# Performance work log

Hardware: AMD Instinct MI355X
Metric: run time of the kernel (lower is better)

Reference implementation:

```python
import jax, jax.numpy as jnp
import numpy as np

D = 512; H = 8; NL = 8; V = 258; W = 8; DFF = 4 * D; DH = D // H


def setup_inputs() -> dict:
    key = jax.random.key(0)
    ks = jax.random.split(key, 20)
    B, L = 8, 1024
    s = 0.02
    n = lambda k, shp: (jax.random.normal(k, shp, jnp.float32) * s)
    x = jax.random.randint(ks[0], (B, L), 0, 256)
    return dict(
        x=x,
        embed=n(ks[1], (V, D)),
        ep_w=n(ks[2], (D, 1)), ep_b=jnp.zeros((D,), jnp.float32),
        in_w=n(ks[3], (NL, 3 * D, D)), in_b=jnp.zeros((NL, 3 * D), jnp.float32),
        op_w=n(ks[4], (NL, D, D)), op_b=jnp.zeros((NL, D), jnp.float32),
        ln1_w=jnp.ones((NL, D), jnp.float32), ln1_b=jnp.zeros((NL, D), jnp.float32),
        ln2_w=jnp.ones((NL, D), jnp.float32), ln2_b=jnp.zeros((NL, D), jnp.float32),
        f1_w=n(ks[5], (NL, DFF, D)), f1_b=jnp.zeros((NL, DFF), jnp.float32),
        f2_w=n(ks[6], (NL, D, DFF)), f2_b=jnp.zeros((NL, D), jnp.float32),
        out_w=n(ks[7], (V, D)),
    )


def _layer_norm(x, w, b, eps=1e-5):
    mu = jnp.mean(x, -1, keepdims=True)
    var = jnp.mean(jnp.square(x - mu), -1, keepdims=True)
    return (x - mu) * jax.lax.rsqrt(var + eps) * w + b


def _entropy_features(x):
    # Sliding-window byte histogram entropy (same math as one-hot.sum over window)
    B, L = x.shape
    oh = jax.nn.one_hot(x, V, dtype=jnp.float32)          # [B,L,V]
    oh = oh.at[..., 256:].set(0.0)                        # special tokens zeroed
    cs = jnp.cumsum(oh, axis=1)
    cs = jnp.concatenate([jnp.zeros_like(cs[:, :1]), cs], axis=1)
    counts = cs[:, W:] - cs[:, :-W]                       # [B, L-W+1, V]
    probs = jnp.clip(counts / W, 1e-10)
    ent = -jnp.sum(probs * (jnp.log(probs) / jnp.log(2.0)), -1, keepdims=True)
    return jnp.pad(ent, ((0, 0), (0, W - 1), (0, 0)))     # [B,L,1]


def _block(h, in_w, in_b, op_w, op_b, ln1_w, ln1_b, ln2_w, ln2_b, f1_w, f1_b, f2_w, f2_b):
    B, L, _ = h.shape
    g = _layer_norm(h, ln1_w, ln1_b)
    qkv = g @ in_w.T + in_b                               # [B,L,3D]
    q, k, v = jnp.split(qkv, 3, axis=-1)
    q = q.reshape(B, L, H, DH); k = k.reshape(B, L, H, DH); v = v.reshape(B, L, H, DH)
    scores = jnp.einsum('blhd,bmhd->bhlm', q, k) / np.sqrt(DH).astype(np.float32)
    attn = jax.nn.softmax(scores, axis=-1)
    o = jnp.einsum('bhlm,bmhd->blhd', attn, v).reshape(B, L, D)
    h = h + o @ op_w.T + op_b
    g = _layer_norm(h, ln2_w, ln2_b)
    h = h + jax.nn.gelu(g @ f1_w.T + f1_b, approximate=False) @ f2_w.T + f2_b
    return h


def reference(x, embed, ep_w, ep_b, in_w, in_b, op_w, op_b, ln1_w, ln1_b,
              ln2_w, ln2_b, f1_w, f1_b, f2_w, f2_b, out_w):
    ent = _entropy_features(x)                            # [B,L,1]
    h = embed[x] + ent @ ep_w.T + ep_b                    # [B,L,D]
    for i in range(NL // 2):                              # local encoder layers
        h = _block(h, in_w[i], in_b[i], op_w[i], op_b[i], ln1_w[i], ln1_b[i],
                   ln2_w[i], ln2_b[i], f1_w[i], f1_b[i], f2_w[i], f2_b[i])
    for i in range(NL // 2, NL):                          # global transformer layers
        h = _block(h, in_w[i], in_b[i], op_w[i], op_b[i], ln1_w[i], ln1_b[i],
                   ln2_w[i], ln2_b[i], f1_w[i], f1_b[i], f2_w[i], f2_b[i])
    return h @ out_w.T                                    # [B,L,V]
```

## Files before the change

### kernel.cpp

```cpp
#include <hip/hip_runtime.h>
#include <hip/hip_bf16.h>

#define D_MODEL 512
#define NHEAD   8
#define DHEAD   64
#define SEQ     1024
#define NBATCH  8
#define NTOK    8192
#define DFF_N   2048
#define NLAYER  8
#define VOCAB   258
#define VPAD    384

typedef float f32x4 __attribute__((ext_vector_type(4)));
typedef short s16x8 __attribute__((ext_vector_type(8)));

__device__ __forceinline__ ushort f2b(float f) {
    union { float f; unsigned u; } v; v.f = f;
    unsigned r = (v.u + 0x7fffu + ((v.u >> 16) & 1u)) >> 16;
    return (ushort)r;
}
__device__ __forceinline__ float gelu_f(float x) {
    return 0.5f * x * (1.0f + erff(x * 0.70710678118654752f));
}
__device__ __forceinline__ void gl_lds16(const void* g, void* l) {
    __builtin_amdgcn_global_load_lds(
        (const __attribute__((address_space(1))) void*)g,
        (__attribute__((address_space(3))) void*)l, 16, 0, 0);
}
__device__ __forceinline__ float exp2_fast(float x) {
    float r; asm("v_exp_f32 %0, %1" : "=v"(r) : "v"(x)); return r;
}
__device__ __forceinline__ unsigned cvtpk(float lo, float hi) {
    unsigned r; asm("v_cvt_pk_bf16_f32 %0, %1, %2" : "=v"(r) : "v"(lo), "v"(hi)); return r;
}

__global__ __launch_bounds__(256) void cvt_bf16(
    const float* __restrict__ in, ushort* __restrict__ out, int n)
{
    int i = (blockIdx.x * 256 + threadIdx.x) << 2;
    if (i >= n) return;
    float4 v = *(const float4*)(in + i);
    ushort4 o;
    o.x = f2b(v.x); o.y = f2b(v.y); o.z = f2b(v.z); o.w = f2b(v.w);
    *(ushort4*)(out + i) = o;
}

__global__ __launch_bounds__(256) void cvt_layer(
    const float* __restrict__ s0, const float* __restrict__ s1,
    const float* __restrict__ s2, const float* __restrict__ s3,
    ushort* __restrict__ d0, ushort* __restrict__ d1,
    ushort* __restrict__ d2, ushort* __restrict__ d3)
{
    int i = (blockIdx.x * 256 + threadIdx.x) << 2;
    const float* s; ushort* d; int off;
    if (i < 786432)        { s = s0; d = d0; off = i; }
    else if (i < 1048576)  { s = s1; d = d1; off = i - 786432; }
    else if (i < 2097152)  { s = s2; d = d2; off = i - 1048576; }
    else                   { s = s3; d = d3; off = i - 2097152; }
    float4 v = *(const float4*)(s + off);
    ushort4 o;
    o.x = f2b(v.x); o.y = f2b(v.y); o.z = f2b(v.z); o.w = f2b(v.w);
    *(ushort4*)(d + off) = o;
}

__global__ __launch_bounds__(128) void embed_kernel(
    const int* __restrict__ x, const float* __restrict__ embed,
    const float* __restrict__ ep_w, const float* __restrict__ ep_b,
    float* __restrict__ h)
{
    int t = blockIdx.x;
    int pos = t & (SEQ - 1);
    float ent = 0.0f;
    if (pos <= SEQ - 8) {
        int v[8];
        #pragma unroll
        for (int i = 0; i < 8; i++) v[i] = x[t + i];
        float s = 0.0f;
        #pragma unroll
        for (int i = 0; i < 8; i++) {
            int c = 0;
            #pragma unroll
            for (int j = 0; j < 8; j++) c += (v[j] == v[i]) ? 1 : 0;
            s += log2f((float)c);
        }
        ent = 3.0f - 0.125f * s;
    }
    int tok = x[t];
    int d = threadIdx.x << 2;
    float e[4], w[4], bb[4], r[4];
    *(float4*)e  = *(const float4*)(embed + (size_t)tok * D_MODEL + d);
    *(float4*)w  = *(const float4*)(ep_w + d);
    *(float4*)bb = *(const float4*)(ep_b + d);
    #pragma unroll
    for (int j = 0; j < 4; j++) r[j] = e[j] + ent * w[j] + bb[j];
    *(float4*)(h + (size_t)t * D_MODEL + d) = *(float4*)r;
}

__global__ __launch_bounds__(256) void ln_kernel(
    const float* __restrict__ in, const float* __restrict__ w,
    const float* __restrict__ b, ushort* __restrict__ out)
{
    int wid = threadIdx.x >> 6, lane = threadIdx.x & 63;
    int t = (blockIdx.x << 2) + wid;
    const float* row = in + (size_t)t * D_MODEL;
    float a[8];
    *(float4*)(a)     = *(const float4*)(row + (lane << 2));
    *(float4*)(a + 4) = *(const float4*)(row + 256 + (lane << 2));
    float s = 0.f;
    #pragma unroll
    for (int j = 0; j < 8; j++) s += a[j];
    #pragma unroll
    for (int o = 1; o < 64; o <<= 1) s += __shfl_xor(s, o);
    float mu = s * (1.0f / 512.0f);
    float vs = 0.f;
    #pragma unroll
    for (int j = 0; j < 8; j++) { float d0 = a[j] - mu; vs += d0 * d0; }
    #pragma unroll
    for (int o = 1; o < 64; o <<= 1) vs += __shfl_xor(vs, o);
    float inv = rsqrtf(vs * (1.0f / 512.0f) + 1e-5f);
    float ww[8], bbv[8];
    *(float4*)(ww)      = *(const float4*)(w + (lane << 2));
    *(float4*)(ww + 4)  = *(const float4*)(w + 256 + (lane << 2));
    *(float4*)(bbv)     = *(const float4*)(b + (lane << 2));
    *(float4*)(bbv + 4) = *(const float4*)(b + 256 + (lane << 2));
    ushort* orow = out + (size_t)t * D_MODEL;
    ushort4 o1, o2;
    o1.x = f2b((a[0] - mu) * inv * ww[0] + bbv[0]);
    o1.y = f2b((a[1] - mu) * inv * ww[1] + bbv[1]);
    o1.z = f2b((a[2] - mu) * inv * ww[2] + bbv[2]);
    o1.w = f2b((a[3] - mu) * inv * ww[3] + bbv[3]);
    o2.x = f2b((a[4] - mu) * inv * ww[4] + bbv[4]);
    o2.y = f2b((a[5] - mu) * inv * ww[5] + bbv[5]);
    o2.z = f2b((a[6] - mu) * inv * ww[6] + bbv[6]);
    o2.w = f2b((a[7] - mu) * inv * ww[7] + bbv[7]);
    *(ushort4*)(orow + (lane << 2))       = o1;
    *(ushort4*)(orow + 256 + (lane << 2)) = o2;
}

template<int BN>
__global__ __launch_bounds__(256) void gemm_t(
    const ushort* __restrict__ A, const ushort* __restrict__ Bw,
    const float* __restrict__ bias, const float* __restrict__ resid,
    float* __restrict__ Cf, ushort* __restrict__ Cb, ushort* __restrict__ Vtr,
    int M, int N, int K, int fuse)
{
    constexpr int NF = BN / 32;
    constexpr int EPW = BN + 4;
    __shared__ ushort SMEM[3 * 4096 + 3 * BN * 32];
    ushort* As0 = SMEM;
    ushort* Bs0 = SMEM + 12288;
    const int tid = threadIdx.x;
    const int l = tid & 63, w = tid >> 6;
    const int p  = blockIdx.y * gridDim.x + blockIdx.x;
    const int bx = ((p & 7) << 3) + ((p >> 3) & 7);
    const int by = p >> 6;
    const int m0 = bx << 7, n0 = by * BN;
    const int wrn = (w >> 1) << 6;
    const int wcn = (w & 1) * (BN / 2);
    const int fm = l & 15;
    const int soff = (((l & 3) ^ ((l >> 3) & 3)) << 3);
    const int foff = (((l >> 4) ^ ((fm >> 1) & 3)) << 3);
    f32x4 acc[4][NF] = {};

    const ushort* ga0 = A + (size_t)(m0 + (w << 5) + (l >> 2)) * K + soff;
    const ushort* ga1 = ga0 + (size_t)16 * K;
    const ushort* gb0;
    const ushort* gb1 = nullptr;
    if constexpr (BN == 128) {
        gb0 = Bw + (size_t)(n0 + (w << 5) + (l >> 2)) * K + soff;
        gb1 = gb0 + (size_t)16 * K;
    } else {
        gb0 = Bw + (size_t)(n0 + (w << 4) + (l >> 2)) * K + soff;
    }

    const int nk = K >> 5;
    auto stage = [&](int buf, int ko) {
        gl_lds16(ga0 + ko, As0 + buf * 4096 + (w << 10));
        gl_lds16(ga1 + ko, As0 + buf * 4096 + (w << 10) + 512);
        if constexpr (BN == 128) {
            gl_lds16(gb0 + ko, Bs0 + buf * (BN * 32) + (w << 10));
            gl_lds16(gb1 + ko, Bs0 + buf * (BN * 32) + (w << 10) + 512);
        } else {
            gl_lds16(gb0 + ko, Bs0 + buf * (BN * 32) + (w << 9));
        }
    };

    stage(0, 0);
    stage(1, 32);
    int cur = 0;
    for (int kt = 0; kt < nk; ++kt) {
        if (kt + 1 < nk) {
            if constexpr (BN == 128) asm volatile("s_waitcnt vmcnt(4)" ::: "memory");
            else                     asm volatile("s_waitcnt vmcnt(3)" ::: "memory");
        } else {
            asm volatile("s_waitcnt vmcnt(0)" ::: "memory");
        }
        asm volatile("s_barrier" ::: "memory");
        __builtin_amdgcn_sched_barrier(0);
        {
            int nxt = cur + 2; if (nxt >= 3) nxt -= 3;
            if (kt + 2 < nk) stage(nxt, (kt + 2) << 5);
        }
        s16x8 af[4], bf[NF];
        #pragma unroll
        for (int x = 0; x < 4; ++x)
            af[x] = *(const s16x8*)&As0[cur * 4096 + (wrn + (x << 4) + fm) * 32 + foff];
        #pragma unroll
        for (int y = 0; y < NF; ++y)
            bf[y] = *(const s16x8*)&Bs0[cur * (BN * 32) + (wcn + (y << 4) + fm) * 32 + foff];
        #pragma unroll
        for (int x = 0; x < 4; ++x)
            #pragma unroll
            for (int y = 0; y < NF; ++y)
                acc[x][y] = __builtin_amdgcn_mfma_f32_16x16x32_bf16(
                    af[x], bf[y], acc[x][y], 0, 0, 0);
        cur = (cur == 2) ? 0 : cur + 1;
    }
    __syncthreads();

    const float qs = (Vtr && n0 < 512) ? 0.18033688011112042f : 1.0f;
    const bool vblk = (Vtr != nullptr) && (n0 >= 1024);

    if (Cb != nullptr || vblk) {
        float* Ep = (float*)SMEM;
        const int lrw = ((w >> 1) << 4) + ((l >> 4) << 2);
        #pragma unroll
        for (int x = 0; x < 4; ++x) {
            __syncthreads();
            #pragma unroll
            for (int y = 0; y < NF; ++y) {
                const int c = wcn + (y << 4) + fm;
                const float bv = bias ? bias[n0 + c] : 0.f;
                #pragma unroll
                for (int i = 0; i < 4; ++i) {
                    float v = acc[x][y][i] + bv;
                    v *= qs;
                    if (fuse == 1) v = gelu_f(v);
                    Ep[(lrw + i) * EPW + c] = v;
                }
            }
            __syncthreads();
            if (vblk) {
                const int c = tid & 127;
                const int run = tid >> 7;
                const int colg = (n0 - 1024) + c;
                const int hh = colg >> 6, dd = colg & 63;
                float v16[16];
                #pragma unroll
                for (int j = 0; j < 16; ++j)
                    v16[j] = Ep[((run << 4) + j) * EPW + c];
                unsigned pk[8];
                #pragma unroll
                for (int j = 0; j < 8; ++j) pk[j] = cvtpk(v16[2 * j], v16[2 * j + 1]);
                ushort* dst = Vtr + ((size_t)(((m0 >> 10) << 3) + hh) * 64 + dd) * 1024
                              + (m0 & 1023) + (run << 6) + (x << 4);
                *(uint4*)dst       = *(uint4*)(pk);
                *(uint4*)(dst + 8) = *(uint4*)(pk + 4);
            } else {
                constexpr int TPR = BN / 8;
                constexpr int RPP = 256 / TPR;
                constexpr int NP = 32 / RPP;
                #pragma unroll
                for (int p2 = 0; p2 < NP; ++p2) {
                    const int lr = p2 * RPP + (tid / TPR);
                    const int cg = (tid % TPR) << 3;
                    const int grow = m0 + ((lr >> 4) << 6) + (x << 4) + (lr & 15);
                    const int gcol = n0 + cg;
                    float v8[8];
                    *(float4*)(v8)     = *(float4*)&Ep[lr * EPW + cg];
                    *(float4*)(v8 + 4) = *(float4*)&Ep[lr * EPW + cg + 4];
                    if (fuse == 2) {
                        float4 r1 = *(const float4*)&resid[(size_t)grow * N + gcol];
                        float4 r2 = *(const float4*)&resid[(size_t)grow * N + gcol + 4];
                        v8[0] += r1.x; v8[1] += r1.y; v8[2] += r1.z; v8[3] += r1.w;
                        v8[4] += r2.x; v8[5] += r2.y; v8[6] += r2.z; v8[7] += r2.w;
                    }
                    if (Cf) {
                        *(float4*)&Cf[(size_t)grow * N + gcol]     = *(float4*)v8;
                        *(float4*)&Cf[(size_t)grow * N + gcol + 4] = *(float4*)(v8 + 4);
                    }
                    unsigned pk[4];
                    pk[0] = cvtpk(v8[0], v8[1]); pk[1] = cvtpk(v8[2], v8[3]);
                    pk[2] = cvtpk(v8[4], v8[5]); pk[3] = cvtpk(v8[6], v8[7]);
                    *(uint4*)&Cb[(size_t)grow * N + gcol] = *(uint4*)pk;
                }
            }
        }
        return;
    }

    const int col0 = n0 + wcn + fm;
    const int row0 = m0 + wrn + ((l >> 4) << 2);
    #pragma unroll
    for (int x = 0; x < 4; ++x) {
        #pragma unroll
        for (int y = 0; y < NF; ++y) {
            int col = col0 + (y << 4);
            if (col >= N) continue;
            float bv = bias ? bias[col] : 0.f;
            #pragma unroll
            for (int i = 0; i < 4; ++i) {
                int row = row0 + (x << 4) + i;
                float v = acc[x][y][i] + bv;
                if (fuse == 1) v = gelu_f(v);
                else if (fuse == 2) v += resid[(size_t)row * N + col];
                Cf[(size_t)row * N + col] = v;
            }
        }
    }
}

__global__ __launch_bounds__(512) void attn_mfma(
    const ushort* __restrict__ qkv, const ushort* __restrict__ vT,
    ushort* __restrict__ out)
{
    __shared__ ushort Ks[2][4096];
    __shared__ ushort Vs[2][4096];
    const int tid = threadIdx.x;
    const int l = tid & 63, w = tid >> 6;
    const int p = blockIdx.y * gridDim.x + blockIdx.x;
    const int bh = ((p & 7) << 3) + (p >> 6);
    const int q0 = ((p >> 3) & 7) << 7;
    const int b = bh >> 3, h = bh & 7;
    const ushort* base = qkv + (size_t)b * SEQ * 1536 + h * 64;
    const ushort* kg = base + 512;
    const ushort* vg = vT + ((size_t)bh << 16);
    const int fm = l & 15, fk = l >> 4;

    s16x8 qf[2];
    {
        const ushort* qrow = base + (size_t)(q0 + (w << 4) + fm) * 1536 + (fk << 3);
        qf[0] = *(const s16x8*)qrow;
        qf[1] = *(const s16x8*)(qrow + 32);
    }
    s16x8 ones_f;
    #pragma unroll
    for (int j = 0; j < 8; ++j) ones_f[j] = (short)0x3F80;

    f32x4 accO[4] = {};
    f32x4 accL = {};

    const int srow = (w << 3) + (l >> 3);
    const int cch = ((l & 7) ^ (l >> 3)) << 3;
    const ushort* kga = kg + (size_t)srow * 1536 + cch;
    const ushort* vga = vg + (size_t)srow * 1024 + cch;

    int fidx[2][4];
    #pragma unroll
    for (int ks = 0; ks < 2; ++ks)
        #pragma unroll
        for (int n = 0; n < 4; ++n)
            fidx[ks][n] = (((n << 4) + fm) << 6) + ((((ks << 2) + fk) ^ (l & 7)) << 3);

    const int srcA = ((fk & 1) << 5) + fm;
    const int srcB = srcA + 16;
    const bool hiN = (fk >> 1) != 0;

    #define STAGE(buf, kt)                                                    \
        do {                                                                  \
            gl_lds16(kga + (size_t)((kt) << 6) * 1536, &Ks[buf][w << 9]);     \
            gl_lds16(vga + ((kt) << 6), &Vs[buf][w << 9]);                    \
        } while (0)

    STAGE(0, 0);
    asm volatile("s_waitcnt vmcnt(0)" ::: "memory");
    __builtin_amdgcn_s_barrier();

    int cur = 0;
    for (int kt = 0; kt < SEQ / 64; ++kt) {
        if (kt + 1 < SEQ / 64) STAGE(cur ^ 1, kt + 1);
        __builtin_amdgcn_sched_barrier(0);

        f32x4 s[4] = {};
        __builtin_amdgcn_s_setprio(1);
        #pragma unroll
        for (int ks = 0; ks < 2; ++ks)
            #pragma unroll
            for (int n = 0; n < 4; ++n) {
                s16x8 kf = *(const s16x8*)&Ks[cur][fidx[ks][n]];
                s[n] = __builtin_amdgcn_mfma_f32_16x16x32_bf16(kf, qf[ks], s[n], 0, 0, 0);
            }
        __builtin_amdgcn_s_setprio(0);

        unsigned pk0[2], pk1[2], pk2[2], pk3[2];
        pk0[0] = cvtpk(exp2_fast(s[0][0]), exp2_fast(s[0][1]));
        pk0[1] = cvtpk(exp2_fast(s[0][2]), exp2_fast(s[0][3]));
        pk1[0] = cvtpk(exp2_fast(s[1][0]), exp2_fast(s[1][1]));
        pk1[1] = cvtpk(exp2_fast(s[1][2]), exp2_fast(s[1][3]));
        pk2[0] = cvtpk(exp2_fast(s[2][0]), exp2_fast(s[2][1]));
        pk2[1] = cvtpk(exp2_fast(s[2][2]), exp2_fast(s[2][3]));
        pk3[0] = cvtpk(exp2_fast(s[3][0]), exp2_fast(s[3][1]));
        pk3[1] = cvtpk(exp2_fast(s[3][2]), exp2_fast(s[3][3]));

        #pragma unroll
        for (int ks = 0; ks < 2; ++ks) {
            unsigned u0 = ks ? pk2[0] : pk0[0], u1 = ks ? pk2[1] : pk0[1];
            unsigned v0 = ks ? pk3[0] : pk1[0], v1 = ks ? pk3[1] : pk1[1];
            unsigned a0 = __shfl((int)u0, srcA), b0 = __shfl((int)v0, srcA);
            unsigned a1 = __shfl((int)u1, srcA), b1 = __shfl((int)v1, srcA);
            unsigned a2 = __shfl((int)u0, srcB), b2 = __shfl((int)v0, srcB);
            unsigned a3 = __shfl((int)u1, srcB), b3 = __shfl((int)v1, srcB);
            union { unsigned u[4]; s16x8 v; } pb;
            pb.u[0] = hiN ? b0 : a0;
            pb.u[1] = hiN ? b1 : a1;
            pb.u[2] = hiN ? b2 : a2;
            pb.u[3] = hiN ? b3 : a3;
            __builtin_amdgcn_s_setprio(1);
            #pragma unroll
            for (int n = 0; n < 4; ++n) {
                s16x8 vf = *(const s16x8*)&Vs[cur][fidx[ks][n]];
                accO[n] = __builtin_amdgcn_mfma_f32_16x16x32_bf16(vf, pb.v, accO[n], 0, 0, 0);
            }
            accL = __builtin_amdgcn_mfma_f32_16x16x32_bf16(ones_f, pb.v, accL, 0, 0, 0);
            __builtin_amdgcn_s_setprio(0);
        }

        asm volatile("s_waitcnt vmcnt(0)" ::: "memory");
        __builtin_amdgcn_s_barrier();
        __builtin_amdgcn_sched_barrier(0);
        cur ^= 1;
    }
    #undef STAGE

    const int q = q0 + (w << 4) + fm;
    float inv = 1.0f / accL[0];
    ushort* obase = out + ((size_t)(b * SEQ + q)) * 512 + h * 64 + (fk << 2);
    #pragma unroll
    for (int n = 0; n < 4; ++n) {
        ushort4 o;
        o.x = f2b(accO[n][0] * inv);
        o.y = f2b(accO[n][1] * inv);
        o.z = f2b(accO[n][2] * inv);
        o.w = f2b(accO[n][3] * inv);
        *(ushort4*)(obase + (n << 4)) = o;
    }
}

extern "C" void kernel_launch(void* const* d_in, const int* in_sizes, int n_in,
                              void* d_out, int out_size, void* d_ws, size_t ws_size,
                              hipStream_t stream) {
    const int*   x     = (const int*)  d_in[0];
    const float* embed = (const float*)d_in[1];
    const float* ep_w  = (const float*)d_in[2];
    const float* ep_b  = (const float*)d_in[3];
    const float* in_w  = (const float*)d_in[4];
    const float* in_b  = (const float*)d_in[5];
    const float* op_w  = (const float*)d_in[6];
    const float* op_b  = (const float*)d_in[7];
    const float* ln1_w = (const float*)d_in[8];
    const float* ln1_b = (const float*)d_in[9];
    const float* ln2_w = (const float*)d_in[10];
    const float* ln2_b = (const float*)d_in[11];
    const float* f1_w  = (const float*)d_in[12];
    const float* f1_b  = (const float*)d_in[13];
    const float* f2_w  = (const float*)d_in[14];
    const float* f2_b  = (const float*)d_in[15];
    const float* out_w = (const float*)d_in[16];
    float* out = (float*)d_out;

    char* ws = (char*)d_ws;
    float*  h    = (float*) (ws + 0);
    ushort* g    = (ushort*)(ws + 16777216);
    ushort* big  = (ushort*)(ws + 25165824);
    ushort* qkvb = big;
    ushort* hb   = (ushort*)(ws + 58720256);
    ushort* wq   = (ushort*)(ws + 67108864);
    ushort* wo   = (ushort*)(ws + 68681728);
    ushort* w1   = (ushort*)(ws + 69206016);
    ushort* w2   = (ushort*)(ws + 71303168);
    ushort* wv   = (ushort*)(ws + 73400320);
    ushort* vT   = (ushort*)(ws + 73793536);

    hipMemsetAsync(wv, 0, (size_t)VPAD * 512 * 2, stream);
    cvt_bf16<<<(VOCAB * 512 / 4 + 255) / 256, 256, 0, stream>>>(out_w, wv, VOCAB * 512);

    embed_kernel<<<NTOK, 128, 0, stream>>>(x, embed, ep_w, ep_b, h);

    for (int l = 0; l < NLAYER; ++l) {
        cvt_layer<<<3072, 256, 0, stream>>>(
            in_w + (size_t)l * 786432, op_w + (size_t)l * 262144,
            f1_w + (size_t)l * 1048576, f2_w + (size_t)l * 1048576,
            wq, wo, w1, w2);

        ln_kernel<<<NTOK / 4, 256, 0, stream>>>(h, ln1_w + l * 512, ln1_b + l * 512, g);
        gemm_t<128><<<dim3(64, 12), 256, 0, stream>>>(g, wq, in_b + l * 1536, nullptr,
                                                      nullptr, qkvb, vT, NTOK, 1536, 512, 0);
        attn_mfma<<<dim3(SEQ / 128, 64), 512, 0, stream>>>(qkvb, vT, g);
        gemm_t<64><<<dim3(64, 8), 256, 0, stream>>>(g, wo, op_b + l * 512, h,
                                                    h, nullptr, nullptr, NTOK, 512, 512, 2);
        ln_kernel<<<NTOK / 4, 256, 0, stream>>>(h, ln2_w + l * 512, ln2_b + l * 512, g);
        gemm_t<128><<<dim3(64, 16), 256, 0, stream>>>(g, w1, f1_b + l * 2048, nullptr,
                                                      nullptr, big, nullptr, NTOK, 2048, 512, 1);
        gemm_t<64><<<dim3(64, 8), 256, 0, stream>>>(big, w2, f2_b + l * 512, h,
                                                    h, (l == NLAYER - 1) ? hb : nullptr, nullptr,
                                                    NTOK, 512, 2048, 2);
    }

    gemm_t<64><<<dim3(64, 5), 256, 0, stream>>>(hb, wv, nullptr, nullptr,
                                                out, nullptr, nullptr, NTOK, VOCAB, 512, 0);
}
```

Before: 1.351 ms.

## Add triple-buffered BK=64 GEMM kernel for N=512 projections and output head

Introduces a new 128x64-tile GEMM that stages 64-wide K slices into a three-deep LDS ring with async global-to-LDS loads and XOR-swizzled addressing. Each barrier now covers two MFMA k-steps, and loads run two tiles ahead. It replaces the older 64-variant GEMM for the attention out-projection, the FFN down-projection and the vocab head. The bf16 output path stages results through LDS for vectorized stores. The cost is more LDS per block, which may reduce occupancy.

After: 1.297 ms, median of 2. -4.0%, faster.

```diff
diff --git a/kernel.cpp b/kernel.cpp
--- a/kernel.cpp
+++ b/kernel.cpp
@@ -311,6 +311,159 @@
     }
 }
 
+__global__ __launch_bounds__(256) void gemm_k64(
+    const ushort* __restrict__ A, const ushort* __restrict__ Bw,
+    const float* __restrict__ bias, const float* __restrict__ resid,
+    float* __restrict__ Cf, ushort* __restrict__ Cb,
+    int M, int N, int K, int fuse)
+{
+    constexpr int EPW = 68;
+    __shared__ ushort SMEM[3 * 8192 + 3 * 4096];
+    ushort* As0 = SMEM;
+    ushort* Bs0 = SMEM + 24576;
+    const int tid = threadIdx.x;
+    const int l = tid & 63, w = tid >> 6;
+    const int p  = blockIdx.y * gridDim.x + blockIdx.x;
+    const int bx = ((p & 7) << 3) + ((p >> 3) & 7);
+    const int by = p >> 6;
+    const int m0 = bx << 7, n0 = by << 6;
+    const int wrn = (w >> 1) << 6;
+    const int wcn = (w & 1) << 5;
+    const int fm = l & 15, fk = l >> 4;
+    f32x4 acc[4][2] = {};
+
+    const int srow = (w << 3) + (l >> 3);
+    const int cch = ((l & 7) ^ (l >> 3)) << 3;
+    const ushort* gaP0 = A + (size_t)(m0 + srow) * K + cch;
+    const ushort* gbP0 = Bw + (size_t)(n0 + srow) * K + cch;
+
+    const int foff0 = (((0 << 2) + fk) ^ (fm & 7)) << 3;
+    const int foff1 = (((1 << 2) + fk) ^ (fm & 7)) << 3;
+
+    const int nk = K >> 6;
+    auto stage = [&](int buf, int ko) {
+        #pragma unroll
+        for (int p2 = 0; p2 < 4; ++p2)
+            gl_lds16(gaP0 + (size_t)(p2 << 5) * K + ko,
+                     As0 + buf * 8192 + (p2 << 11) + (w << 9));
+        #pragma unroll
+        for (int p2 = 0; p2 < 2; ++p2)
+            gl_lds16(gbP0 + (size_t)(p2 << 5) * K + ko,
+                     Bs0 + buf * 4096 + (p2 << 11) + (w << 9));
+    };
+
+    stage(0, 0);
+    stage(1, 64);
+    int cur = 0;
+    for (int kt = 0; kt < nk; ++kt) {
+        if (kt + 1 < nk) asm volatile("s_waitcnt vmcnt(6)" ::: "memory");
+        else             asm volatile("s_waitcnt vmcnt(0)" ::: "memory");
+        asm volatile("s_barrier" ::: "memory");
+        __builtin_amdgcn_sched_barrier(0);
+        {
+            int nxt = cur + 2; if (nxt >= 3) nxt -= 3;
+            if (kt + 2 < nk) stage(nxt, (kt + 2) << 6);
+        }
+        {
+            s16x8 af[4], bf[2];
+            #pragma unroll
+            for (int x = 0; x < 4; ++x)
+                af[x] = *(const s16x8*)&As0[cur * 8192 + (wrn + (x << 4) + fm) * 64 + foff0];
+            #pragma unroll
+            for (int y = 0; y < 2; ++y)
+                bf[y] = *(const s16x8*)&Bs0[cur * 4096 + (wcn + (y << 4) + fm) * 64 + foff0];
+            #pragma unroll
+            for (int x = 0; x < 4; ++x)
+                #pragma unroll
+                for (int y = 0; y < 2; ++y)
+                    acc[x][y] = __builtin_amdgcn_mfma_f32_16x16x32_bf16(
+                        af[x], bf[y], acc[x][y], 0, 0, 0);
+        }
+        {
+            s16x8 af[4], bf[2];
+            #pragma unroll
+            for (int x = 0; x < 4; ++x)
+                af[x] = *(const s16x8*)&As0[cur * 8192 + (wrn + (x << 4) + fm) * 64 + foff1];
+            #pragma unroll
+            for (int y = 0; y < 2; ++y)
+                bf[y] = *(const s16x8*)&Bs0[cur * 4096 + (wcn + (y << 4) + fm) * 64 + foff1];
+            #pragma unroll
+            for (int x = 0; x < 4; ++x)
+                #pragma unroll
+                for (int y = 0; y < 2; ++y)
+                    acc[x][y] = __builtin_amdgcn_mfma_f32_16x16x32_bf16(
+                        af[x], bf[y], acc[x][y], 0, 0, 0);
+        }
+        cur = (cur == 2) ? 0 : cur + 1;
+    }
+    __syncthreads();
+
+    if (Cb != nullptr) {
+        float* Ep = (float*)SMEM;
+        const int lrw = ((w >> 1) << 4) + ((l >> 4) << 2);
+        #pragma unroll
+        for (int x = 0; x < 4; ++x) {
+            __syncthreads();
+            #pragma unroll
+            for (int y = 0; y < 2; ++y) {
+                const int c = wcn + (y << 4) + fm;
+                const float bv = bias ? bias[n0 + c] : 0.f;
+                #pragma unroll
+                for (int i = 0; i < 4; ++i) {
+                    float v = acc[x][y][i] + bv;
+                    if (fuse == 1) v = gelu_f(v);
+                    Ep[(lrw + i) * EPW + c] = v;
+                }
+            }
+            __syncthreads();
+            {
+                const int lr = tid >> 3;
+                const int cg = (tid & 7) << 3;
+                const int grow = m0 + ((lr >> 4) << 6) + (x << 4) + (lr & 15);
+                const int gcol = n0 + cg;
+                float v8[8];
+                *(float4*)(v8)     = *(float4*)&Ep[lr * EPW + cg];
+                *(float4*)(v8 + 4) = *(float4*)&Ep[lr * EPW + cg + 4];
+                if (fuse == 2) {
+                    float4 r1 = *(const float4*)&resid[(size_t)grow * N + gcol];
+                    float4 r2 = *(const float4*)&resid[(size_t)grow * N + gcol + 4];
+                    v8[0] += r1.x; v8[1] += r1.y; v8[2] += r1.z; v8[3] += r1.w;
+                    v8[4] += r2.x; v8[5] += r2.y; v8[6] += r2.z; v8[7] += r2.w;
+                }
+                if (Cf) {
+                    *(float4*)&Cf[(size_t)grow * N + gcol]     = *(float4*)v8;
+                    *(float4*)&Cf[(size_t)grow * N + gcol + 4] = *(float4*)(v8 + 4);
+                }
+                unsigned pk[4];
+                pk[0] = cvtpk(v8[0], v8[1]); pk[1] = cvtpk(v8[2], v8[3]);
+                pk[2] = cvtpk(v8[4], v8[5]); pk[3] = cvtpk(v8[6], v8[7]);
+                *(uint4*)&Cb[(size_t)grow * N + gcol] = *(uint4*)pk;
+            }
+        }
+        return;
+    }
+
+    const int col0 = n0 + wcn + fm;
+    const int row0 = m0 + wrn + ((l >> 4) << 2);
+    #pragma unroll
+    for (int x = 0; x < 4; ++x) {
+        #pragma unroll
+        for (int y = 0; y < 2; ++y) {
+            int col = col0 + (y << 4);
+            if (col >= N) continue;
+            float bv = bias ? bias[col] : 0.f;
+            #pragma unroll
+            for (int i = 0; i < 4; ++i) {
+                int row = row0 + (x << 4) + i;
+                float v = acc[x][y][i] + bv;
+                if (fuse == 1) v = gelu_f(v);
+                else if (fuse == 2) v += resid[(size_t)row * N + col];
+                Cf[(size_t)row * N + col] = v;
+            }
+        }
+    }
+}
+
 __global__ __launch_bounds__(512) void attn_mfma(
     const ushort* __restrict__ qkv, const ushort* __restrict__ vT,
     ushort* __restrict__ out)
@@ -487,16 +640,16 @@
         gemm_t<128><<<dim3(64, 12), 256, 0, stream>>>(g, wq, in_b + l * 1536, nullptr,
                                                       nullptr, qkvb, vT, NTOK, 1536, 512, 0);
         attn_mfma<<<dim3(SEQ / 128, 64), 512, 0, stream>>>(qkvb, vT, g);
-        gemm_t<64><<<dim3(64, 8), 256, 0, stream>>>(g, wo, op_b + l * 512, h,
-                                                    h, nullptr, nullptr, NTOK, 512, 512, 2);
+        gemm_k64<<<dim3(64, 8), 256, 0, stream>>>(g, wo, op_b + l * 512, h,
+                                                  h, nullptr, NTOK, 512, 512, 2);
         ln_kernel<<<NTOK / 4, 256, 0, stream>>>(h, ln2_w + l * 512, ln2_b + l * 512, g);
         gemm_t<128><<<dim3(64, 16), 256, 0, stream>>>(g, w1, f1_b + l * 2048, nullptr,
                                                       nullptr, big, nullptr, NTOK, 2048, 512, 1);
-        gemm_t<64><<<dim3(64, 8), 256, 0, stream>>>(big, w2, f2_b + l * 512, h,
-                                                    h, (l == NLAYER - 1) ? hb : nullptr, nullptr,
-                                                    NTOK, 512, 2048, 2);
-    }
-
-    gemm_t<64><<<dim3(64, 5), 256, 0, stream>>>(hb, wv, nullptr, nullptr,
-                                                out, nullptr, nullptr, NTOK, VOCAB, 512, 0);
-}
+        gemm_k64<<<dim3(64, 8), 256, 0, stream>>>(big, w2, f2_b + l * 512, h,
+                                                  h, (l == NLAYER - 1) ? hb : nullptr,
+                                                  NTOK, 512, 2048, 2);
+    }
+
+    gemm_k64<<<dim3(64, 5), 256, 0, stream>>>(hb, wv, nullptr, nullptr,
+                                              out, nullptr, NTOK, VOCAB, 512, 0);
+}
```
